# Kernel tuning notes

Measured on AMD Instinct MI355X. Metric: run time of the kernel, lower is better.

The kernel has to match this reference:

```python
import jax, jax.numpy as jnp
import numpy as np

N = 50000        # nodes
E = 800000       # edges
FEAT = 64        # cfg.feature_dim
HID = 128        # cfg.hidden_dim
G = 8            # num graphs
EPS = 1e-5       # LayerNorm eps
MIN_DEPTH, MAX_DEPTH = 0.1, 3.0


def _ln(x, g, b):
    m = jnp.mean(x, axis=-1, keepdims=True)
    v = jnp.mean((x - m) ** 2, axis=-1, keepdims=True)
    return (x - m) * jax.lax.rsqrt(v + EPS) * g + b


def setup_inputs() -> dict:
    key = jax.random.key(0)
    ks = jax.random.split(key, 32)
    f32 = jnp.float32
    inp = {}
    inp['x'] = jax.random.normal(ks[0], (N, FEAT), dtype=f32)
    inp['edge_index'] = jax.random.randint(ks[1], (2, E), 0, N)
    inp['batch'] = jnp.sort(jax.random.randint(ks[2], (N,), 0, G))
    # input_projection: Linear(FEAT,HID) + LayerNorm
    inp['in_w'] = jax.random.normal(ks[3], (FEAT, HID), dtype=f32) * (1.0 / np.sqrt(FEAT))
    inp['in_b'] = jnp.zeros((HID,), f32)
    inp['in_ln_g'] = jnp.ones((HID,), f32)
    inp['in_ln_b'] = jnp.zeros((HID,), f32)
    # epigenetics
    inp['methylation'] = jnp.zeros((HID,), f32)
    inp['histones'] = jnp.zeros((4,), f32)
    inp['log_depth'] = jnp.zeros((), f32)
    # NeuralODEFunc: 3 stacked GCNConv(HID,HID) + LayerNorms, gate MLP, residual scalar
    inp['gcn_w'] = jax.random.normal(ks[4], (3, HID, HID), dtype=f32) * (1.0 / np.sqrt(HID))
    inp['gcn_b'] = jnp.zeros((3, HID), f32)
    inp['ln_g'] = jnp.ones((3, HID), f32)
    inp['ln_b'] = jnp.zeros((3, HID), f32)
    inp['gate_w'] = jax.random.normal(ks[5], (2 * HID, HID), dtype=f32) * (1.0 / np.sqrt(2 * HID))
    inp['gate_b'] = jnp.zeros((HID,), f32)
    inp['residual_weight'] = jnp.asarray(0.1, f32)
    # output_projection: Linear(HID,HID) + LayerNorm
    inp['out_w'] = jax.random.normal(ks[6], (HID, HID), dtype=f32) * (1.0 / np.sqrt(HID))
    inp['out_b'] = jnp.zeros((HID,), f32)
    inp['out_ln_g'] = jnp.ones((HID,), f32)
    inp['out_ln_b'] = jnp.zeros((HID,), f32)
    return inp


def reference(x, edge_index, batch, in_w, in_b, in_ln_g, in_ln_b, methylation,
              histones, log_depth, gcn_w, gcn_b, ln_g, ln_b, gate_w, gate_b,
              residual_weight, out_w, out_b, out_ln_g, out_ln_b):
    n = x.shape[0]
    src, dst = edge_index[0], edge_index[1]

    # input_projection (Dropout is identity in eval)
    h = jax.nn.relu(_ln(x @ in_w + in_b, in_ln_g, in_ln_b))

    # epigenetic regulation (chromatin_accessibility goes through .item() -> constant)
    meth_sil = jnp.mean(jax.nn.sigmoid(methylation))
    hm = jax.nn.sigmoid(histones)
    act = (hm[0] + hm[2]) * 0.5
    rep = (hm[1] + hm[3]) * 0.5
    chrom = jax.lax.stop_gradient(jnp.clip(act - rep + 0.5, 0.0, 1.0))
    h = h * (chrom * (1.0 - meth_sil))

    # symmetric GCN normalization, no self loops (computed once, no grad path)
    deg = jax.ops.segment_sum(jnp.ones((E,), h.dtype), dst, num_segments=n)
    dinv = jnp.where(deg > 0, jax.lax.rsqrt(jnp.maximum(deg, 1.0)), 0.0)
    enorm = (dinv[src] * dinv[dst])[:, None]  # [E,1]

    def gcn(hh, i):
        xw = hh @ gcn_w[i]                                   # [N,H]
        agg = jax.ops.segment_sum(xw[src] * enorm, dst, num_segments=n)
        return agg + gcn_b[i]

    def ode_f(hh):
        h_orig = hh
        cur = hh
        for i in range(3):  # fixed layer count
            h_new = _ln(gcn(cur, i), ln_g[i], ln_b[i])
            if i > 0:
                gate = jax.nn.sigmoid(
                    jnp.concatenate([cur, h_new], axis=-1) @ gate_w + gate_b)
                cur = gate * h_new + (1.0 - gate) * cur
            else:
                cur = h_new
        cur = jnp.tanh(cur)
        return cur + residual_weight * h_orig

    # depth via .item() in torch -> non-differentiable constant
    depth = jax.lax.stop_gradient(
        jnp.clip(jnp.exp(log_depth), MIN_DEPTH, MAX_DEPTH))
    # single fixed RK4 step over t = linspace(0, depth, 2)
    dt = depth
    k1 = ode_f(h)
    k2 = ode_f(h + 0.5 * dt * k1)
    k3 = ode_f(h + 0.5 * dt * k2)
    k4 = ode_f(h + dt * k3)
    h_final = h + (dt / 6.0) * (k1 + 2.0 * k2 + 2.0 * k3 + k4)

    # output_projection + global_mean_pool over batch
    h_out = _ln(h_final @ out_w + out_b, out_ln_g, out_ln_b)
    cnt = jax.ops.segment_sum(jnp.ones((n,), h.dtype), batch, num_segments=G)
    pooled = jax.ops.segment_sum(h_out, batch, num_segments=G)
    return pooled / jnp.maximum(cnt, 1.0)[:, None]
```

## Files before the change

kernel.cpp:

```cpp
#include <hip/hip_runtime.h>
#include <math.h>

#define NN 50000
#define EE 800000
#define HH 128
#define FF 64
#define GG 8
#define PB 500
#define SB 1600

using short8 = __attribute__((ext_vector_type(8))) short;
using f32x4  = __attribute__((ext_vector_type(4))) float;
using f32x2  = __attribute__((ext_vector_type(2))) float;

__device__ __forceinline__ float sigm(float x){ return 1.0f/(1.0f+expf(-x)); }
__device__ __forceinline__ unsigned short f2bf(float f){
    union { float f; unsigned u; } v; v.f = f;
    unsigned r = v.u + 0x7fff + ((v.u >> 16) & 1);
    return (unsigned short)(r >> 16);
}
__device__ __forceinline__ float bf2f(unsigned short h){
    union { unsigned u; float f; } v; v.u = ((unsigned)h) << 16;
    return v.f;
}

#if __has_builtin(__builtin_amdgcn_cvt_pk_fp8_f32) && __has_builtin(__builtin_amdgcn_cvt_pk_f32_fp8)
#define FP8_HW 1
#else
#define FP8_HW 0
#endif

__device__ __forceinline__ unsigned fp8enc1_sw(float f){
    union { float fl; unsigned u; } x; x.fl = f;
    unsigned s = (x.u >> 31) << 7;
    float a = fabsf(f);
    if (!(a > 0.f)) return s;
    if (a >= 448.f) return s | 0x7E;
    if (a < 0.015625f) {
        int q = (int)(a * 512.f + 0.5f);
        if (q > 7) return s | (1u << 3);
        return s | (unsigned)q;
    }
    unsigned u = x.u + (1u << 19);
    int e32 = (int)((u >> 23) & 255) - 127;
    if (e32 < -6) { int q=(int)(a*512.f+0.5f); if(q>7)q=7; return s|(unsigned)q; }
    if (e32 > 8) return s | 0x7E;
    unsigned m = (u >> 20) & 7;
    return s | ((unsigned)(e32 + 7) << 3) | m;
}
__device__ __forceinline__ float fp8dec1_sw(unsigned v){
    unsigned s = v >> 7, e = (v >> 3) & 15, m = v & 7;
    float f;
    if (e == 0) f = (float)m * 0.001953125f;
    else { union { unsigned u; float fl; } x; x.u = ((e + 120u) << 23) | (m << 20); f = x.fl; }
    return s ? -f : f;
}
__device__ __forceinline__ unsigned char e2fp8(float a){
#if FP8_HW
    return (unsigned char)(__builtin_amdgcn_cvt_pk_fp8_f32(a, a, 0, false) & 0xFF);
#else
    return (unsigned char)fp8enc1_sw(a);
#endif
}
__device__ __forceinline__ unsigned pk4fp8(float a, float b, float c, float d){
#if FP8_HW
    unsigned p0 = (unsigned)__builtin_amdgcn_cvt_pk_fp8_f32(a, b, 0, false);
    unsigned p1 = (unsigned)__builtin_amdgcn_cvt_pk_fp8_f32(c, d, 0, false);
    return (p0 & 0xFFFFu) | ((p1 & 0xFFFFu) << 16);
#else
    return fp8enc1_sw(a) | (fp8enc1_sw(b) << 8) | (fp8enc1_sw(c) << 16) | (fp8enc1_sw(d) << 24);
#endif
}
__device__ __forceinline__ float2 d2fp8(unsigned short u){
#if FP8_HW
    f32x2 r = __builtin_amdgcn_cvt_pk_f32_fp8((int)(unsigned)u, false);
    return make_float2(r[0], r[1]);
#else
    return make_float2(fp8dec1_sw(u & 0xFF), fp8dec1_sw((u >> 8) & 0xFF));
#endif
}

__global__ void k_setup(const float* __restrict__ meth,
                        const float* __restrict__ histones,
                        const float* __restrict__ logd,
                        float* __restrict__ scal,
                        const int* __restrict__ batch, int* __restrict__ st)
{
    if (blockIdx.x == 1) {
        int g = threadIdx.x;
        if (g > GG) return;
        int lo = 0, hi = NN;
        while (lo < hi) { int mid = (lo + hi) >> 1; if (batch[mid] < g) lo = mid + 1; else hi = mid; }
        st[g] = lo;
        return;
    }
    int l = threadIdx.x;
    float s = sigm(meth[l]) + sigm(meth[l + 64]);
#pragma unroll
    for (int o = 32; o >= 1; o >>= 1) s += __shfl_xor(s, o, 64);
    if (l == 0) {
        float msil = s * (1.0f / 128.0f);
        float h0 = sigm(histones[0]), h1 = sigm(histones[1]);
        float h2 = sigm(histones[2]), h3 = sigm(histones[3]);
        float act = (h0 + h2) * 0.5f, rep = (h1 + h3) * 0.5f;
        float chrom = fminf(fmaxf(act - rep + 0.5f, 0.0f), 1.0f);
        scal[0] = chrom * (1.0f - msil);
        float d = expf(logd[0]);
        scal[1] = fminf(fmaxf(d, 0.1f), 3.0f);
    }
}

__global__ void k_packall(const float* __restrict__ in_w, const float* __restrict__ gcn_w,
                          const float* __restrict__ gate_w, const float* __restrict__ out_w,
                          unsigned short* __restrict__ outp)
{
    int i = blockIdx.x * 256 + threadIdx.x;
    if (i >= 8192 + 6 * 16384) return;
    const float* src; int base, li;
    if (i < 8192) { src = in_w + i; base = 0; li = i; }
    else {
        int j = i - 8192;
        int m = j >> 14, r = j & 16383;
        base = 8192 + (m << 14); li = r;
        if (m < 3)      src = gcn_w  + m * 16384 + r;
        else if (m < 5) src = gate_w + (m - 3) * 16384 + r;
        else            src = out_w + r;
    }
    int k = li >> 7, n = li & 127;
    int c = k >> 5, kl = k & 31, q = kl >> 3, j2 = kl & 7;
    int b = n >> 4, ln = n & 15;
    int lane = q * 16 + ln;
    outp[base + ((c * 8 + b) * 64 + lane) * 8 + j2] = f2bf(*src);
}

__global__ void k_cvtx(const float* __restrict__ x, unsigned short* __restrict__ xb)
{
    size_t i = (size_t)blockIdx.x * 256 + threadIdx.x;
    if (i >= (size_t)NN * 16) return;
    float4 v = ((const float4*)x)[i];
    ushort4 o;
    o.x = f2bf(v.x); o.y = f2bf(v.y); o.z = f2bf(v.z); o.w = f2bf(v.w);
    ((ushort4*)xb)[i] = o;
}

__global__ void k_hist(const int* __restrict__ ei, int* __restrict__ hist)
{
    int e = blockIdx.x * 256 + threadIdx.x;
    if (e < EE) atomicAdd(&hist[ei[EE + e]], 1);
}

__global__ void k_dinv(const int* __restrict__ hist, float* __restrict__ dinv)
{
    int n = blockIdx.x * 256 + threadIdx.x;
    if (n < NN) {
        int d = hist[n];
        dinv[n] = d > 0 ? rsqrtf((float)d) : 0.0f;
    }
}

__global__ void k_scan_a(const int* __restrict__ hist, int* __restrict__ aux)
{
    __shared__ int sh[256];
    int b = blockIdx.x, t = threadIdx.x;
    int base = b * 1024 + t * 4;
    int s = 0;
#pragma unroll
    for (int j = 0; j < 4; ++j) { int i = base + j; if (i < NN) s += hist[i]; }
    sh[t] = s; __syncthreads();
    for (int o = 128; o >= 1; o >>= 1) { if (t < o) sh[t] += sh[t + o]; __syncthreads(); }
    if (t == 0) aux[b] = sh[0];
}

__global__ void k_scan_b(int* __restrict__ aux, int nb)
{
    if (blockIdx.x == 0 && threadIdx.x == 0) {
        int run = 0;
        for (int i = 0; i < nb; ++i) { int v = aux[i]; aux[i] = run; run += v; }
    }
}

__global__ void k_scan_c(const int* __restrict__ hist, const int* __restrict__ aux,
                         int* __restrict__ row_ptr)
{
    __shared__ int sh[256];
    int b = blockIdx.x, t = threadIdx.x;
    int base = b * 1024 + t * 4;
    int v[4]; int s = 0;
#pragma unroll
    for (int j = 0; j < 4; ++j) { int i = base + j; v[j] = (i < NN) ? hist[i] : 0; s += v[j]; }
    sh[t] = s; __syncthreads();
    for (int o = 1; o < 256; o <<= 1) {
        int x = 0; if (t >= o) x = sh[t - o];
        __syncthreads(); sh[t] += x; __syncthreads();
    }
    int run = aux[b] + sh[t] - s;
#pragma unroll
    for (int j = 0; j < 4; ++j) { int i = base + j; if (i < NN) row_ptr[i] = run; run += v[j]; }
    if (b == 0 && t == 0) row_ptr[NN] = EE;
}

__global__ __launch_bounds__(256) void k_scatter(const int* __restrict__ ei,
                          const float* __restrict__ dinv,
                          int* __restrict__ cursor, uint2* __restrict__ ew)
{
    if (blockIdx.x == 0 && threadIdx.x < 32)
        ew[EE + threadIdx.x] = make_uint2(0u, 0u);
    const int grp = blockIdx.x & 7;
    const int blk = blockIdx.x >> 3;
    const int CH  = EE / (SB / 8);
    const int e0 = blk * CH, e1 = e0 + CH;
    const int glo = grp * (NN / 8), ghi = glo + (NN / 8);
    for (int e = e0 + threadIdx.x; e < e1; e += 256) {
        int d = ei[EE + e];
        if (d >= glo && d < ghi) {
            int s = ei[e];
            int p = atomicAdd(&cursor[d], 1);
            ew[p] = make_uint2((unsigned)(s & 0xFFFF) | ((unsigned)(d & 15) << 16),
                               __float_as_uint(dinv[s] * dinv[d]));
        }
    }
}

template<int KC, int MODE>
__global__ __launch_bounds__(256) void k_dense_mfma(
    const unsigned short* __restrict__ A, const unsigned short* __restrict__ Wp,
    const float* __restrict__ bias, const float* __restrict__ lng,
    const float* __restrict__ lnb, const float* __restrict__ scal,
    unsigned short* __restrict__ out, unsigned char* __restrict__ out8)
{
    __shared__ unsigned short Ws[KC * 4096];
    const int t = threadIdx.x;
    {
        const float4* src = (const float4*)Wp;
        float4* dst = (float4*)Ws;
#pragma unroll
        for (int i = 0; i < KC * 2; ++i) dst[t + i * 256] = src[t + i * 256];
    }
    __syncthreads();
    const int wave = t >> 6, lane = t & 63;
    const int quad = lane >> 4, ln = lane & 15;
    const int r0 = blockIdx.x * 64 + wave * 16;
    const int K = KC * 32;
    const int arow = r0 + ln;
    const bool av = arow < NN;

    f32x4 acc[8] = {};
#pragma unroll
    for (int c = 0; c < KC; ++c) {
        short8 a = {};
        if (av) a = *(const short8*)(A + (size_t)arow * K + c * 32 + quad * 8);
#pragma unroll
        for (int b = 0; b < 8; ++b) {
            short8 bb = *(const short8*)&Ws[((c * 8 + b) * 64 + lane) * 8];
            acc[b] = __builtin_amdgcn_mfma_f32_16x16x32_bf16(a, bb, acc[b], 0, 0, 0);
        }
    }

    float b_s[8], g_s[8], e_s[8];
#pragma unroll
    for (int b = 0; b < 8; ++b) {
        int col = b * 16 + ln;
        b_s[b] = bias[col]; g_s[b] = lng[col]; e_s[b] = lnb[col];
    }
    float sc = (MODE == 1) ? scal[0] : 0.0f;
#pragma unroll
    for (int i = 0; i < 4; ++i) {
        int row = r0 + quad * 4 + i;
        float v[8]; float s = 0.f, q = 0.f;
#pragma unroll
        for (int b = 0; b < 8; ++b) { float x = acc[b][i] + b_s[b]; v[b] = x; s += x; q += x * x; }
#pragma unroll
        for (int o = 1; o < 16; o <<= 1) { s += __shfl_xor(s, o, 64); q += __shfl_xor(q, o, 64); }
        float m  = s * (1.0f / 128.0f);
        float vr = q * (1.0f / 128.0f) - m * m;
        float rs = rsqrtf(vr + 1e-5f);
        if (row < NN) {
#pragma unroll
            for (int b = 0; b < 8; ++b) {
                float o2 = (v[b] - m) * rs * g_s[b] + e_s[b];
                if (MODE == 1) o2 = fmaxf(o2, 0.f) * sc;
                out[(size_t)row * 128 + b * 16 + ln] = f2bf(o2);
                if (out8) out8[(size_t)row * 128 + b * 16 + ln] = e2fp8(o2);
            }
        }
    }
}

__global__ __launch_bounds__(128) void k_spgemm(
    const int* __restrict__ rp, const uint2* __restrict__ ew,
    const unsigned char* __restrict__ X8, const unsigned short* __restrict__ Wp,
    const float* __restrict__ bias, const float* __restrict__ lng,
    const float* __restrict__ lnb, unsigned short* __restrict__ out,
    unsigned char* __restrict__ out8)
{
    __shared__ float accf[16 * 132];
    const int t = threadIdx.x, wave = t >> 6, lane = t & 63;
    const int quad = lane >> 4, ln = lane & 15;
    const int n0 = blockIdx.x * 16;
    const int nf = n0 + wave * 8;

    {
        float* z = accf + wave * 8 * 132;
        for (int i = lane; i < 8 * 132; i += 64) z[i] = 0.f;
    }

    if (nf < NN) {
        const int nl = min(nf + 8, NN);
        const int ebeg = __builtin_amdgcn_readfirstlane(rp[nf]);
        const int eend = __builtin_amdgcn_readfirstlane(rp[nl]);
        if (ebeg < eend) {
            float2 r0a = make_float2(0.f, 0.f), r1a = make_float2(0.f, 0.f);
            int curd = (int)((ew[ebeg].x >> 16) & 15u);
            const unsigned char* Xl = X8 + lane * 2;
            uint2 recA[8], recB[8]; float2 gA[8];
#pragma unroll
            for (int u = 0; u < 8; ++u) recA[u] = ew[ebeg + u];
#pragma unroll
            for (int u = 0; u < 8; ++u) recB[u] = ew[ebeg + 8 + u];
#pragma unroll
            for (int u = 0; u < 8; ++u) {
                int src = (int)(recA[u].x & 0xFFFFu);
                gA[u] = d2fp8(*(const unsigned short*)(Xl + (size_t)src * 128));
            }
            for (int e = ebeg; e < eend; e += 8) {
                float2 gB[8];
#pragma unroll
                for (int u = 0; u < 8; ++u) {
                    int src = (int)(recB[u].x & 0xFFFFu);
                    gB[u] = d2fp8(*(const unsigned short*)(Xl + (size_t)src * 128));
                }
                uint2 recC[8];
#pragma unroll
                for (int u = 0; u < 8; ++u) recC[u] = ew[e + 16 + u];
                const int m = min(8, eend - e);
#pragma unroll
                for (int u = 0; u < 8; ++u) {
                    if (u >= m) break;
                    int dl = (int)((recA[u].x >> 16) & 15u);
                    float wt = __uint_as_float(recA[u].y);
                    if (dl != curd) {
                        *(float2*)&accf[curd * 132 + lane * 2] =
                            make_float2(r0a.x + r1a.x, r0a.y + r1a.y);
                        r0a = make_float2(0.f, 0.f);
                        r1a = make_float2(0.f, 0.f);
                        curd = dl;
                    }
                    if (u & 1) {
                        r1a.x = fmaf(wt, gA[u].x, r1a.x);
                        r1a.y = fmaf(wt, gA[u].y, r1a.y);
                    } else {
                        r0a.x = fmaf(wt, gA[u].x, r0a.x);
                        r0a.y = fmaf(wt, gA[u].y, r0a.y);
                    }
                }
#pragma unroll
                for (int u = 0; u < 8; ++u) { recA[u] = recB[u]; recB[u] = recC[u]; gA[u] = gB[u]; }
            }
            *(float2*)&accf[curd * 132 + lane * 2] =
                make_float2(r0a.x + r1a.x, r0a.y + r1a.y);
        }
    }
    __syncthreads();

    f32x4 acc[8] = {};
    const float* ar = accf + (size_t)ln * 132;
#pragma unroll
    for (int c = 0; c < 4; ++c) {
        float4 a0 = *(const float4*)(ar + c * 32 + quad * 8);
        float4 a1 = *(const float4*)(ar + c * 32 + quad * 8 + 4);
        short8 af;
        af[0] = (short)f2bf(a0.x); af[1] = (short)f2bf(a0.y);
        af[2] = (short)f2bf(a0.z); af[3] = (short)f2bf(a0.w);
        af[4] = (short)f2bf(a1.x); af[5] = (short)f2bf(a1.y);
        af[6] = (short)f2bf(a1.z); af[7] = (short)f2bf(a1.w);
#pragma unroll
        for (int b = 0; b < 8; ++b) {
            short8 bb = *(const short8*)(Wp + ((size_t)(c * 8 + b) * 64 + lane) * 8);
            acc[b] = __builtin_amdgcn_mfma_f32_16x16x32_bf16(af, bb, acc[b], 0, 0, 0);
        }
    }

    float b_s[8], g_s[8], e_s[8];
#pragma unroll
    for (int b = 0; b < 8; ++b) {
        int col = b * 16 + ln;
        b_s[b] = bias[col]; g_s[b] = lng[col]; e_s[b] = lnb[col];
    }
#pragma unroll
    for (int i = 0; i < 4; ++i) {
        int row = n0 + quad * 4 + i;
        float v[8]; float s = 0.f, q = 0.f;
#pragma unroll
        for (int b = 0; b < 8; ++b) { float x = acc[b][i] + b_s[b]; v[b] = x; s += x; q += x * x; }
#pragma unroll
        for (int o = 1; o < 16; o <<= 1) { s += __shfl_xor(s, o, 64); q += __shfl_xor(q, o, 64); }
        float m  = s * (1.0f / 128.0f);
        float vr = q * (1.0f / 128.0f) - m * m;
        float rs = rsqrtf(vr + 1e-5f);
        if (((quad >> 1) == wave) && row < NN) {
#pragma unroll
            for (int b = 0; b < 8; ++b) {
                float o2 = (v[b] - m) * rs * g_s[b] + e_s[b];
                out[(size_t)row * 128 + b * 16 + ln] = f2bf(o2);
                if (out8) out8[(size_t)row * 128 + b * 16 + ln] = e2fp8(o2);
            }
        }
    }
}

__global__ __launch_bounds__(256) void k_gate_mfma(
    unsigned short* __restrict__ cur, const unsigned short* __restrict__ hnew,
    const unsigned short* __restrict__ Wp, const float* __restrict__ gb,
    unsigned char* __restrict__ cur8)
{
    __shared__ unsigned short Ws[16384];
    const int t = threadIdx.x;
    const int wave = t >> 6, lane = t & 63;
    const int quad = lane >> 4, ln = lane & 15;
    const int r0 = blockIdx.x * 64 + wave * 16;
    const int arow = r0 + ln;
    const bool av = arow < NN;

    f32x4 acc[8] = {};
#pragma unroll
    for (int s = 0; s < 2; ++s) {
        __syncthreads();
        {
            const float4* src = (const float4*)(Wp + (size_t)s * 16384);
            float4* dst = (float4*)Ws;
#pragma unroll
            for (int i = 0; i < 8; ++i) dst[t + i * 256] = src[t + i * 256];
        }
        __syncthreads();
        const unsigned short* A = s ? hnew : cur;
#pragma unroll
        for (int c = 0; c < 4; ++c) {
            short8 a = {};
            if (av) a = *(const short8*)(A + (size_t)arow * 128 + c * 32 + quad * 8);
#pragma unroll
            for (int b = 0; b < 8; ++b) {
                short8 bb = *(const short8*)&Ws[((c * 8 + b) * 64 + lane) * 8];
                acc[b] = __builtin_amdgcn_mfma_f32_16x16x32_bf16(a, bb, acc[b], 0, 0, 0);
            }
        }
    }

    float gb_s[8];
#pragma unroll
    for (int b = 0; b < 8; ++b) gb_s[b] = gb[b * 16 + ln];
#pragma unroll
    for (int i = 0; i < 4; ++i) {
        int row = r0 + quad * 4 + i;
        if (row < NN) {
#pragma unroll
            for (int b = 0; b < 8; ++b) {
                size_t idx = (size_t)row * 128 + b * 16 + ln;
                float g  = sigm(acc[b][i] + gb_s[b]);
                float cu = bf2f(cur[idx]);
                float hn = bf2f(hnew[idx]);
                float r  = g * hn + (1.f - g) * cu;
                cur[idx]  = f2bf(r);
                cur8[idx] = e2fp8(r);
            }
        }
    }
}

template<int S>
__global__ __launch_bounds__(256) void k_stage(
    const unsigned short* __restrict__ cur, const unsigned short* __restrict__ fin,
    const unsigned short* __restrict__ h0, float* __restrict__ acc,
    unsigned short* __restrict__ ybuf, const float* __restrict__ scal,
    const float* __restrict__ rwp, unsigned char* __restrict__ y8)
{
    size_t i = (size_t)blockIdx.x * 256 + threadIdx.x;
    if (i >= (size_t)NN * 32) return;
    float dt = scal[1], rw = rwp[0];
    float wk = (S == 1 || S == 4) ? dt * (1.f / 6.f) : dt * (1.f / 3.f);
    ushort4 c4 = ((const ushort4*)cur)[i];
    ushort4 f4 = ((const ushort4*)fin)[i];
    ushort4 h4 = ((const ushort4*)h0)[i];
    float tv[4];
    tv[0] = tanhf(bf2f(c4.x)) + rw * bf2f(f4.x);
    tv[1] = tanhf(bf2f(c4.y)) + rw * bf2f(f4.y);
    tv[2] = tanhf(bf2f(c4.z)) + rw * bf2f(f4.z);
    tv[3] = tanhf(bf2f(c4.w)) + rw * bf2f(f4.w);
    float4 a;
    if (S == 1) { a.x = wk*tv[0]; a.y = wk*tv[1]; a.z = wk*tv[2]; a.w = wk*tv[3]; }
    else {
        a = ((const float4*)acc)[i];
        a.x += wk*tv[0]; a.y += wk*tv[1]; a.z += wk*tv[2]; a.w += wk*tv[3];
    }
    ((float4*)acc)[i] = a;
    float h[4] = { bf2f(h4.x), bf2f(h4.y), bf2f(h4.z), bf2f(h4.w) };
    float yv[4];
    if (S == 4) {
        yv[0] = h[0] + a.x; yv[1] = h[1] + a.y; yv[2] = h[2] + a.z; yv[3] = h[3] + a.w;
    } else {
        float cn = (S == 3) ? dt : 0.5f * dt;
        yv[0] = h[0] + cn*tv[0]; yv[1] = h[1] + cn*tv[1];
        yv[2] = h[2] + cn*tv[2]; yv[3] = h[3] + cn*tv[3];
    }
    ushort4 y;
    y.x = f2bf(yv[0]); y.y = f2bf(yv[1]); y.z = f2bf(yv[2]); y.w = f2bf(yv[3]);
    ((ushort4*)ybuf)[i] = y;
    ((unsigned*)y8)[i] = pk4fp8(yv[0], yv[1], yv[2], yv[3]);
}

__global__ __launch_bounds__(128) void k_pool1(
    const unsigned short* __restrict__ h, const int* __restrict__ batch,
    float* __restrict__ partial)
{
    int c = threadIdx.x, b = blockIdx.x;
    int r0 = b * (NN / PB), r1 = r0 + (NN / PB);
    float acc = 0.f;
    int gfirst = batch[r0], g = gfirst;
#pragma unroll 4
    for (int r = r0; r < r1; ++r) {
        int gg = batch[r];
        if (gg != g) {
            partial[(size_t)b * 1024 + g * 128 + c] = acc;
            for (int z = g + 1; z < gg; ++z) partial[(size_t)b * 1024 + z * 128 + c] = 0.f;
            acc = 0.f; g = gg;
        }
        acc += bf2f(h[(size_t)r * 128 + c]);
    }
    partial[(size_t)b * 1024 + g * 128 + c] = acc;
    for (int z = 0; z < gfirst; ++z)  partial[(size_t)b * 1024 + z * 128 + c] = 0.f;
    for (int z = g + 1; z < GG; ++z)  partial[(size_t)b * 1024 + z * 128 + c] = 0.f;
}

__global__ __launch_bounds__(256) void k_pool2(
    const float* __restrict__ partial, const int* __restrict__ st,
    float* __restrict__ out)
{
    __shared__ float sh[8][32];
    int cb = blockIdx.x & 3, g = blockIdx.x >> 2;
    int cl = threadIdx.x & 31, sl = threadIdx.x >> 5;
    int c = cb * 32 + cl;
    float s = 0.f;
    for (int b = sl; b < PB; b += 8) s += partial[(size_t)b * 1024 + g * 128 + c];
    sh[sl][cl] = s; __syncthreads();
    if (sl == 0) {
        float tt = 0.f;
#pragma unroll
        for (int i = 0; i < 8; ++i) tt += sh[i][cl];
        int cnt = st[g + 1] - st[g];
        out[g * 128 + c] = tt / (float)(cnt > 0 ? cnt : 1);
    }
}

static inline size_t al(size_t x) { return (x + 255) & ~(size_t)255; }

extern "C" void kernel_launch(void* const* d_in, const int* in_sizes, int n_in,
                              void* d_out, int out_size, void* d_ws, size_t ws_size,
                              hipStream_t stream)
{
    const float* x       = (const float*)d_in[0];
    const int*   ei      = (const int*)d_in[1];
    const int*   batch   = (const int*)d_in[2];
    const float* in_w    = (const float*)d_in[3];
    const float* in_b    = (const float*)d_in[4];
    const float* in_lng  = (const float*)d_in[5];
    const float* in_lnb  = (const float*)d_in[6];
    const float* meth    = (const float*)d_in[7];
    const float* histn   = (const float*)d_in[8];
    const float* logd    = (const float*)d_in[9];
    const float* gcn_w   = (const float*)d_in[10];
    const float* gcn_b   = (const float*)d_in[11];
    const float* ln_g    = (const float*)d_in[12];
    const float* ln_b    = (const float*)d_in[13];
    const float* gate_w  = (const float*)d_in[14];
    const float* gate_b  = (const float*)d_in[15];
    const float* rw      = (const float*)d_in[16];
    const float* out_w   = (const float*)d_in[17];
    const float* out_b   = (const float*)d_in[18];
    const float* out_lng = (const float*)d_in[19];
    const float* out_lnb = (const float*)d_in[20];
    float* out = (float*)d_out;

    char* w = (char*)d_ws;
    size_t off = 0;
    float* scal   = (float*)(w + off); off += al(16 * 4);
    int*   hist   = (int*)(w + off);   off += al((size_t)NN * 4);
    int*   rp     = (int*)(w + off);   off += al((size_t)(NN + 1) * 4);
    int*   cursor = (int*)(w + off);   off += al((size_t)(NN + 1) * 4);
    int*   aux    = (int*)(w + off);   off += al(64 * 4);
    int*   st     = (int*)(w + off);   off += al(16 * 4);
    float* dinv   = (float*)(w + off); off += al((size_t)NN * 4);
    uint2* ew     = (uint2*)(w + off); off += al((size_t)(EE + 32) * 8);
    float* partial= (float*)(w + off); off += al((size_t)PB * 1024 * 4);
    unsigned short* wpak = (unsigned short*)(w + off); off += al((size_t)(8192 + 6 * 16384) * 2);
    unsigned short* inwp  = wpak;
    unsigned short* gcnwp = wpak + 8192;
    unsigned short* gwp   = wpak + 8192 + 3 * 16384;
    unsigned short* owp   = wpak + 8192 + 5 * 16384;
    size_t B16 = al((size_t)NN * 128 * 2);
    unsigned short* xb  = (unsigned short*)(w + off); off += al((size_t)NN * 64 * 2);
    unsigned short* h0  = (unsigned short*)(w + off); off += B16;
    unsigned short* y   = (unsigned short*)(w + off); off += B16;
    unsigned short* cur = (unsigned short*)(w + off); off += B16;
    unsigned short* t2  = (unsigned short*)(w + off); off += B16;
    float* acc = (float*)(w + off); off += al((size_t)NN * 128 * 4);
    size_t B8 = al((size_t)NN * 128);
    unsigned char* h08  = (unsigned char*)(w + off); off += B8;
    unsigned char* y8   = (unsigned char*)(w + off); off += B8;
    unsigned char* cur8 = (unsigned char*)(w + off); off += B8;
    if (off > ws_size) return;

    hipMemsetAsync(hist, 0, (size_t)NN * 4, stream);

    k_setup<<<2, 64, 0, stream>>>(meth, histn, logd, scal, batch, st);
    k_packall<<<(8192 + 6 * 16384 + 255) / 256, 256, 0, stream>>>(in_w, gcn_w, gate_w, out_w, wpak);
    k_cvtx<<<3125, 256, 0, stream>>>(x, xb);

    k_hist<<<(EE + 255) / 256, 256, 0, stream>>>(ei, hist);
    k_dinv<<<(NN + 255) / 256, 256, 0, stream>>>(hist, dinv);
    k_scan_a<<<49, 256, 0, stream>>>(hist, aux);
    k_scan_b<<<1, 1, 0, stream>>>(aux, 49);
    k_scan_c<<<49, 256, 0, stream>>>(hist, aux, rp);
    hipMemcpyAsync(cursor, rp, (size_t)(NN + 1) * 4, hipMemcpyDeviceToDevice, stream);
    k_scatter<<<SB, 256, 0, stream>>>(ei, dinv, cursor, ew);

    const int DG = (NN + 63) / 64;
    const int SG = (NN + 15) / 16;
    k_dense_mfma<2, 1><<<DG, 256, 0, stream>>>(xb, inwp, in_b, in_lng, in_lnb, scal, h0, h08);

    for (int s = 1; s <= 4; ++s) {
        const unsigned short* fin = (s == 1) ? h0 : y;
        const unsigned char*  fin8 = (s == 1) ? h08 : y8;
        k_spgemm<<<SG, 128, 0, stream>>>(rp, ew, fin8, gcnwp, gcn_b, ln_g, ln_b, cur, cur8);
        for (int i = 1; i <= 2; ++i) {
            k_spgemm<<<SG, 128, 0, stream>>>(rp, ew, cur8,
                                             gcnwp + (size_t)i * 128 * 128, gcn_b + i * 128,
                                             ln_g + i * 128, ln_b + i * 128, t2, (unsigned char*)0);
            k_gate_mfma<<<DG, 256, 0, stream>>>(cur, t2, gwp, gate_b, cur8);
        }
        if (s == 1)      k_stage<1><<<6250, 256, 0, stream>>>(cur, fin, h0, acc, y, scal, rw, y8);
        else if (s == 2) k_stage<2><<<6250, 256, 0, stream>>>(cur, fin, h0, acc, y, scal, rw, y8);
        else if (s == 3) k_stage<3><<<6250, 256, 0, stream>>>(cur, fin, h0, acc, y, scal, rw, y8);
        else             k_stage<4><<<6250, 256, 0, stream>>>(cur, fin, h0, acc, y, scal, rw, y8);
    }

    k_dense_mfma<4, 0><<<DG, 256, 0, stream>>>(y, owp, out_b, out_lng, out_lnb, scal, t2, (unsigned char*)0);
    k_pool1<<<PB, 128, 0, stream>>>(t2, batch, partial);
    k_pool2<<<GG * 4, 256, 0, stream>>>(partial, st, out);
}
```

Before: 901.9 us.

## Split SpMM edge gather across four lane subgroups with wider fp8 loads

Restructures the sparse aggregation so each wave splits into four 16-lane subgroups. Each subgroup handles every fourth edge and each lane loads 8 fp8 features (uint2) instead of 2, so a wave covers 32 edges per iteration. Partial sums from the subgroups are merged into the shared accumulator with LDS atomicAdd when the destination changes, and the edge padding grows to 128 entries to allow the deeper prefetch. The aim is more memory-level parallelism and fewer load instructions per edge, in exchange for LDS atomic traffic and more flushes.

```diff
diff --git a/kernel.cpp b/kernel.cpp
--- a/kernel.cpp
+++ b/kernel.cpp
@@ -203,7 +203,7 @@
                           const float* __restrict__ dinv,
                           int* __restrict__ cursor, uint2* __restrict__ ew)
 {
-    if (blockIdx.x == 0 && threadIdx.x < 32)
+    if (blockIdx.x == 0 && threadIdx.x < 128)
         ew[EE + threadIdx.x] = make_uint2(0u, 0u);
     const int grp = blockIdx.x & 7;
     const int blk = blockIdx.x >> 3;
@@ -296,6 +296,7 @@
     __shared__ float accf[16 * 132];
     const int t = threadIdx.x, wave = t >> 6, lane = t & 63;
     const int quad = lane >> 4, ln = lane & 15;
+    const int sg = quad, li = ln;
     const int n0 = blockIdx.x * 16;
     const int nf = n0 + wave * 8;
 
@@ -309,55 +310,58 @@
         const int ebeg = __builtin_amdgcn_readfirstlane(rp[nf]);
         const int eend = __builtin_amdgcn_readfirstlane(rp[nl]);
         if (ebeg < eend) {
-            float2 r0a = make_float2(0.f, 0.f), r1a = make_float2(0.f, 0.f);
-            int curd = (int)((ew[ebeg].x >> 16) & 15u);
-            const unsigned char* Xl = X8 + lane * 2;
-            uint2 recA[8], recB[8]; float2 gA[8];
-#pragma unroll
-            for (int u = 0; u < 8; ++u) recA[u] = ew[ebeg + u];
-#pragma unroll
-            for (int u = 0; u < 8; ++u) recB[u] = ew[ebeg + 8 + u];
-#pragma unroll
-            for (int u = 0; u < 8; ++u) {
-                int src = (int)(recA[u].x & 0xFFFFu);
-                gA[u] = d2fp8(*(const unsigned short*)(Xl + (size_t)src * 128));
+            float acc8[8] = {};
+            int curd = wave * 8;
+            const unsigned char* Xl = X8 + li * 8;
+            uint2 rec[8], recN[8], g[8];
+#pragma unroll
+            for (int j = 0; j < 8; ++j) rec[j]  = ew[ebeg + 4 * j + sg];
+#pragma unroll
+            for (int j = 0; j < 8; ++j) recN[j] = ew[ebeg + 32 + 4 * j + sg];
+#pragma unroll
+            for (int j = 0; j < 8; ++j) {
+                int src = (int)(rec[j].x & 0xFFFFu);
+                g[j] = *(const uint2*)(Xl + (size_t)src * 128);
             }
-            for (int e = ebeg; e < eend; e += 8) {
-                float2 gB[8];
-#pragma unroll
-                for (int u = 0; u < 8; ++u) {
-                    int src = (int)(recB[u].x & 0xFFFFu);
-                    gB[u] = d2fp8(*(const unsigned short*)(Xl + (size_t)src * 128));
+            for (int e = ebeg; e < eend; e += 32) {
+                uint2 gN[8], recNN[8];
+#pragma unroll
+                for (int j = 0; j < 8; ++j) {
+                    int src = (int)(recN[j].x & 0xFFFFu);
+                    gN[j] = *(const uint2*)(Xl + (size_t)src * 128);
                 }
-                uint2 recC[8];
-#pragma unroll
-                for (int u = 0; u < 8; ++u) recC[u] = ew[e + 16 + u];
-                const int m = min(8, eend - e);
-#pragma unroll
-                for (int u = 0; u < 8; ++u) {
-                    if (u >= m) break;
-                    int dl = (int)((recA[u].x >> 16) & 15u);
-                    float wt = __uint_as_float(recA[u].y);
+#pragma unroll
+                for (int j = 0; j < 8; ++j) recNN[j] = ew[e + 64 + 4 * j + sg];
+                int lim = eend - e - sg;
+                int mj = lim > 0 ? ((lim + 3) >> 2) : 0; if (mj > 8) mj = 8;
+#pragma unroll
+                for (int j = 0; j < 8; ++j) {
+                    if (j >= mj) break;
+                    float wgt = __uint_as_float(rec[j].y);
+                    int dl = (int)((rec[j].x >> 16) & 15u);
                     if (dl != curd) {
-                        *(float2*)&accf[curd * 132 + lane * 2] =
-                            make_float2(r0a.x + r1a.x, r0a.y + r1a.y);
-                        r0a = make_float2(0.f, 0.f);
-                        r1a = make_float2(0.f, 0.f);
+                        float* row = accf + curd * 132 + li * 8;
+#pragma unroll
+                        for (int k = 0; k < 8; ++k) { atomicAdd(&row[k], acc8[k]); acc8[k] = 0.f; }
                         curd = dl;
                     }
-                    if (u & 1) {
-                        r1a.x = fmaf(wt, gA[u].x, r1a.x);
-                        r1a.y = fmaf(wt, gA[u].y, r1a.y);
-                    } else {
-                        r0a.x = fmaf(wt, gA[u].x, r0a.x);
-                        r0a.y = fmaf(wt, gA[u].y, r0a.y);
-                    }
+                    float2 p0 = d2fp8((unsigned short)(g[j].x & 0xFFFFu));
+                    float2 p1 = d2fp8((unsigned short)(g[j].x >> 16));
+                    float2 p2 = d2fp8((unsigned short)(g[j].y & 0xFFFFu));
+                    float2 p3 = d2fp8((unsigned short)(g[j].y >> 16));
+                    acc8[0] = fmaf(wgt, p0.x, acc8[0]); acc8[1] = fmaf(wgt, p0.y, acc8[1]);
+                    acc8[2] = fmaf(wgt, p1.x, acc8[2]); acc8[3] = fmaf(wgt, p1.y, acc8[3]);
+                    acc8[4] = fmaf(wgt, p2.x, acc8[4]); acc8[5] = fmaf(wgt, p2.y, acc8[5]);
+                    acc8[6] = fmaf(wgt, p3.x, acc8[6]); acc8[7] = fmaf(wgt, p3.y, acc8[7]);
                 }
 #pragma unroll
-                for (int u = 0; u < 8; ++u) { recA[u] = recB[u]; recB[u] = recC[u]; gA[u] = gB[u]; }
+                for (int j = 0; j < 8; ++j) { rec[j] = recN[j]; recN[j] = recNN[j]; g[j] = gN[j]; }
             }
-            *(float2*)&accf[curd * 132 + lane * 2] =
-                make_float2(r0a.x + r1a.x, r0a.y + r1a.y);
+            {
+                float* row = accf + curd * 132 + li * 8;
+#pragma unroll
+                for (int k = 0; k < 8; ++k) atomicAdd(&row[k], acc8[k]);
+            }
         }
     }
     __syncthreads();
@@ -588,7 +592,7 @@
     int*   aux    = (int*)(w + off);   off += al(64 * 4);
     int*   st     = (int*)(w + off);   off += al(16 * 4);
     float* dinv   = (float*)(w + off); off += al((size_t)NN * 4);
-    uint2* ew     = (uint2*)(w + off); off += al((size_t)(EE + 32) * 8);
+    uint2* ew     = (uint2*)(w + off); off += al((size_t)(EE + 128) * 8);
     float* partial= (float*)(w + off); off += al((size_t)PB * 1024 * 4);
     unsigned short* wpak = (unsigned short*)(w + off); off += al((size_t)(8192 + 6 * 16384) * 2);
     unsigned short* inwp  = wpak;
```

Result: slower. 2.246 ms (+149.0%).
